# Optimization experiments

Hardware: AMD Instinct MI355X
Metric: run time of the kernel (lower is better)

## Reference

```python
import jax, jax.numpy as jnp
import numpy as np

N = 50000
D_IN = 512
D_HID = 2048
N_CLS = 40
E = 200000


def setup_inputs() -> dict:
    key = jax.random.key(0)
    ks = jax.random.split(key, 8)
    x = jax.random.normal(ks[0], (N, D_IN), dtype=jnp.float32)
    edge_index = jax.random.randint(ks[1], (2, E), 0, N, dtype=jnp.int32)
    # GCNConv weights (glorot-ish scale) and biases
    W1 = jax.random.normal(ks[2], (D_IN, D_HID), dtype=jnp.float32) / np.sqrt(D_IN)
    b1 = jnp.zeros((D_HID,), dtype=jnp.float32)
    W2 = jax.random.normal(ks[3], (D_HID, D_HID), dtype=jnp.float32) / np.sqrt(D_HID)
    b2 = jnp.zeros((D_HID,), dtype=jnp.float32)
    W3 = jax.random.normal(ks[4], (D_HID, N_CLS), dtype=jnp.float32) / np.sqrt(D_HID)
    b3 = jnp.zeros((N_CLS,), dtype=jnp.float32)
    return {"x": x, "edge_index": edge_index, "W1": W1, "b1": b1,
            "W2": W2, "b2": b2, "W3": W3, "b3": b3}


def _gcn_conv(x, src, dst, deg_norm, W, b, n):
    # PyG GCNConv: transform first, then normalized sum-aggregate, then bias.
    h = x @ W                              # [N, out]
    msg = h[src] * deg_norm[:, None]       # [E+N, out] gather + edge normalize
    out = jax.ops.segment_sum(msg, dst, num_segments=n)  # scatter-add
    return out + b


def _pairnorm(x, scale=1.0, eps=1e-6):
    # PyG PairNorm (scale_individually=False): center cols, rescale by mean row norm.
    xc = x - x.mean(axis=0, keepdims=True)
    denom = jnp.sqrt(eps + (xc * xc).sum(axis=-1).mean())
    return scale * xc / denom


def _edges_with_self_loops_and_norm(edge_index, n):
    loop = jnp.arange(n, dtype=edge_index.dtype)
    src = jnp.concatenate([edge_index[0], loop])
    dst = jnp.concatenate([edge_index[1], loop])
    deg = jax.ops.segment_sum(jnp.ones_like(dst, dtype=jnp.float32), dst, num_segments=n)
    dinv = jnp.where(deg > 0, jax.lax.rsqrt(jnp.maximum(deg, 1.0)), 0.0)
    norm = dinv[src] * dinv[dst]           # D^{-1/2} (A+I) D^{-1/2} edge weights
    return src, dst, norm


def reference(x, edge_index, W1, b1, W2, b2, W3, b3):
    n = x.shape[0]
    # drop_edge keep_ratio=1.0 keeps all edges -> identity
    src, dst, norm = _edges_with_self_loops_and_norm(edge_index, n)
    h = _gcn_conv(x, src, dst, norm, W1, b1, n)
    h = jax.nn.relu(_pairnorm(h))
    h = _gcn_conv(h, src, dst, norm, W2, b2, n)
    h = jax.nn.relu(_pairnorm(h))
    out = _gcn_conv(h, src, dst, norm, W3, b3, n)
    return out
```

## Files before the change

kernel.cpp:

```cpp
#include <hip/hip_runtime.h>
#include <cstdint>
#include <cstddef>

using f32x4 = __attribute__((ext_vector_type(4))) float;
using short8 = __attribute__((ext_vector_type(8))) short;

__device__ __forceinline__ float blo(unsigned int u) { return __uint_as_float(u << 16); }
__device__ __forceinline__ float bhi(unsigned int u) { return __uint_as_float(u & 0xffff0000u); }
__device__ __forceinline__ unsigned short f2b(float f) {
  unsigned int i = __float_as_uint(f);
  return (unsigned short)((i + 0x7fffu + ((i >> 16) & 1u)) >> 16);
}
__device__ __forceinline__ unsigned int packb2(float a, float b) {
  return (unsigned int)f2b(a) | ((unsigned int)f2b(b) << 16);
}
__device__ __forceinline__ void gload_lds16(const void* g, void* l) {
  typedef __attribute__((address_space(1))) const unsigned int gui_t;
  typedef __attribute__((address_space(3))) unsigned int lui_t;
  __builtin_amdgcn_global_load_lds((gui_t*)(uintptr_t)g, (lui_t*)(uintptr_t)l, 16, 0, 0);
}
__device__ __forceinline__ void xcd_remap(int gx, int gy, int& bx, int& by) {
  int nwg = gx * gy;
  int flat = by * gx + bx;
  int q = nwg >> 3, rmd = nwg & 7;
  int xcd = flat & 7, pos = flat >> 3;
  int base = (xcd < rmd) ? xcd * (q + 1) : rmd * (q + 1) + (xcd - rmd) * q;
  int nf = base + pos;
  bx = nf % gx;
  by = nf / gx;
}

__global__ void k_sentinel(float* out, long long total, float v) {
  long long i = (long long)blockIdx.x * blockDim.x + threadIdx.x;
  long long stride = (long long)gridDim.x * blockDim.x;
  for (; i < total; i += stride) out[i] = v;
}

__global__ void k_init_deg(int* deg, int n) {
  int i = blockIdx.x * blockDim.x + threadIdx.x;
  if (i < n) deg[i] = 1;
}
__global__ void k_count(const int* __restrict__ ei, int* __restrict__ deg, int e) {
  int i = blockIdx.x * blockDim.x + threadIdx.x;
  if (i < e) atomicAdd(&deg[ei[e + i]], 1);
}
__global__ void k_dinv(const int* __restrict__ deg, float* __restrict__ dinv, int n) {
  int i = blockIdx.x * blockDim.x + threadIdx.x;
  if (i < n) dinv[i] = rsqrtf((float)deg[i]);
}
__global__ void k_scan(const int* __restrict__ deg, int* __restrict__ offs, int n) {
  __shared__ int sums[1024];
  int tid = threadIdx.x;
  int chunk = (n + 1023) / 1024;
  int s0 = tid * chunk, s1 = s0 + chunk;
  if (s1 > n) s1 = n;
  if (s0 > n) s0 = n;
  int s = 0;
  for (int i = s0; i < s1; i++) s += deg[i];
  sums[tid] = s;
  __syncthreads();
  if (tid == 0) {
    int acc = 0;
    for (int i = 0; i < 1024; i++) { int v = sums[i]; sums[i] = acc; acc += v; }
  }
  __syncthreads();
  int off = sums[tid];
  for (int i = s0; i < s1; i++) { offs[i] = off; off += deg[i]; }
  if (tid == 1023) offs[n] = off;
}
__global__ void k_copy_int(int* __restrict__ dst, const int* __restrict__ src, int n) {
  int i = blockIdx.x * blockDim.x + threadIdx.x;
  if (i < n) dst[i] = src[i];
}
__global__ void k_copy_u4(uint4* __restrict__ dst, const uint4* __restrict__ src, int n16) {
  int i = blockIdx.x * blockDim.x + threadIdx.x;
  int stride = gridDim.x * blockDim.x;
  for (; i < n16; i += stride) dst[i] = src[i];
}
__global__ void k_fill_edges(const int* __restrict__ ei, int e, int* __restrict__ cursor,
                             unsigned short* __restrict__ colv) {
  int i = blockIdx.x * blockDim.x + threadIdx.x;
  if (i < e) {
    int s = ei[i], d = ei[e + i];
    int pos = atomicAdd(&cursor[d], 1);
    colv[pos] = (unsigned short)s;
  }
}
__global__ void k_fill_loops(int* __restrict__ cursor, unsigned short* __restrict__ colv, int n) {
  int i = blockIdx.x * blockDim.x + threadIdx.x;
  if (i < n) {
    int pos = atomicAdd(&cursor[i], 1);
    colv[pos] = (unsigned short)i;
  }
}

__global__ void k_transpose_cvt(const float* __restrict__ in, unsigned short* __restrict__ out,
                                int K, int M, int Mout) {
  __shared__ float tile[32][33];
  int kb = blockIdx.x * 32;
  int mb = blockIdx.y * 32;
  int tx = threadIdx.x, ty = threadIdx.y;
#pragma unroll
  for (int j = 0; j < 4; j++) {
    int k = kb + ty + j * 8, m = mb + tx;
    tile[ty + j * 8][tx] = (k < K && m < M) ? in[(size_t)k * M + m] : 0.0f;
  }
  __syncthreads();
#pragma unroll
  for (int j = 0; j < 4; j++) {
    int m = mb + ty + j * 8, k = kb + tx;
    if (m < Mout && k < K) out[(size_t)m * K + k] = f2b(tile[tx][ty + j * 8]);
  }
}

__global__ void k_aggregate_f32(const float* __restrict__ in, unsigned short* __restrict__ out,
                                const int* __restrict__ offs, const unsigned short* __restrict__ colv,
                                const float* __restrict__ dinv) {
  int i = blockIdx.x;
  int tid = threadIdx.x;
  float di = dinv[i];
  int p0 = offs[i], p1 = offs[i + 1];
  const float2* inv = (const float2*)in;
  float a0 = 0.f, a1 = 0.f;
  for (int p = p0; p < p1; p++) {
    int c = (int)colv[p];
    float wgt = dinv[c] * di;
    float2 v = inv[(size_t)c * 256 + tid];
    a0 += wgt * v.x; a1 += wgt * v.y;
  }
  ((unsigned int*)out)[(size_t)i * 256 + tid] = packb2(a0, a1);
}

__global__ void k_aggregate_pn(const unsigned short* __restrict__ in, unsigned short* __restrict__ outws,
                               unsigned short* __restrict__ outtail, int rsplit,
                               const int* __restrict__ offs, const unsigned short* __restrict__ colv,
                               const float* __restrict__ dinv, const float* __restrict__ meanv,
                               const float* __restrict__ scalev) {
  int i = blockIdx.x;
  int tid = threadIdx.x;
  float di = dinv[i];
  float s = scalev[0];
  float m[8];
#pragma unroll
  for (int j = 0; j < 8; j++) m[j] = meanv[tid * 8 + j];
  int p0 = offs[i], p1 = offs[i + 1];
  const uint4* inv = (const uint4*)in;
  float a[8] = {};
  for (int p = p0; p < p1; p++) {
    int c = (int)colv[p];
    float wgt = dinv[c] * di;
    uint4 u = inv[(size_t)c * 256 + tid];
    a[0] += wgt * fmaxf((blo(u.x) - m[0]) * s, 0.f);
    a[1] += wgt * fmaxf((bhi(u.x) - m[1]) * s, 0.f);
    a[2] += wgt * fmaxf((blo(u.y) - m[2]) * s, 0.f);
    a[3] += wgt * fmaxf((bhi(u.y) - m[3]) * s, 0.f);
    a[4] += wgt * fmaxf((blo(u.z) - m[4]) * s, 0.f);
    a[5] += wgt * fmaxf((bhi(u.z) - m[5]) * s, 0.f);
    a[6] += wgt * fmaxf((blo(u.w) - m[6]) * s, 0.f);
    a[7] += wgt * fmaxf((bhi(u.w) - m[7]) * s, 0.f);
  }
  uint4 o;
  o.x = packb2(a[0], a[1]); o.y = packb2(a[2], a[3]);
  o.z = packb2(a[4], a[5]); o.w = packb2(a[6], a[7]);
  char* base = (i < rsplit) ? (char*)outws + (size_t)i * 4096
                            : (char*)outtail + (size_t)(i - rsplit) * 4096;
  ((uint4*)base)[tid] = o;
}

template <int BM, int BN, int WAVES_M, int WAVES_N, bool ADD_BIAS, bool OUT_BF16, bool STATS>
__global__ __launch_bounds__(256) void k_gemm_bf16(const unsigned short* __restrict__ A,
                                                   const char* __restrict__ a_tail, int rsplit,
                                                   const unsigned short* __restrict__ BT,
                                                   const float* __restrict__ bias,
                                                   float* __restrict__ colsum, float* __restrict__ ssq,
                                                   void* __restrict__ Cout,
                                                   int M, int K, int Nout, int m_base) {
  constexpr int BK = 64;
  constexpr int FM = BM / (WAVES_M * 16);
  constexpr int FN = BN / (WAVES_N * 16);
  __shared__ unsigned short lA[BM * BK];
  __shared__ unsigned short lB[BN * BK];
  const int tid = threadIdx.x;
  const int lane = tid & 63;
  const int wid = tid >> 6;
  int bx = blockIdx.x, by = blockIdx.y;
  xcd_remap(gridDim.x, gridDim.y, bx, by);
  const int n0 = bx * BN;
  const int m0 = m_base + by * BM;
  const int wrow = (wid / WAVES_N) * (FM * 16);
  const int wcol = (wid % WAVES_N) * (FN * 16);
  constexpr int ABYTES = BM * BK * 2;
  constexpr int BBYTES = BN * BK * 2;
  constexpr int ACH = ABYTES / 4096;
  constexpr int BCH = BBYTES / 4096;
  const size_t rowbytes = (size_t)K * 2;

  f32x4 acc[FM][FN] = {};

  const int frow = lane & 15;
  const int kcol8 = (lane >> 4) * 8;
  const int xorb = (lane & 7) << 4;

  for (int k0 = 0; k0 < K; k0 += BK) {
#pragma unroll
    for (int c = 0; c < ACH; c++) {
      int o = wid * (ABYTES / 4) + c * 1024 + lane * 16;
      int r = o >> 7;
      int kbs = (o & 127) ^ ((r & 7) << 4);
      int gr = m0 + r; if (gr >= M) gr = M - 1;
      const char* rowp = (gr < rsplit) ? (const char*)A + (size_t)gr * rowbytes
                                       : a_tail + (size_t)(gr - rsplit) * rowbytes;
      gload_lds16(rowp + (size_t)k0 * 2 + kbs, (char*)lA + o);
    }
#pragma unroll
    for (int c = 0; c < BCH; c++) {
      int o = wid * (BBYTES / 4) + c * 1024 + lane * 16;
      int r = o >> 7;
      int kbs = (o & 127) ^ ((r & 7) << 4);
      gload_lds16((const char*)BT + (size_t)(n0 + r) * rowbytes + (size_t)k0 * 2 + kbs, (char*)lB + o);
    }
    __syncthreads();
#pragma unroll
    for (int kk = 0; kk < BK; kk += 32) {
      short8 af[FM], bfr[FN];
#pragma unroll
      for (int t = 0; t < FM; t++)
        af[t] = *(const short8*)((const char*)lA + (wrow + t * 16 + frow) * 128 +
                                 (((kk + kcol8) * 2) ^ xorb));
#pragma unroll
      for (int u = 0; u < FN; u++)
        bfr[u] = *(const short8*)((const char*)lB + (wcol + u * 16 + frow) * 128 +
                                  (((kk + kcol8) * 2) ^ xorb));
#pragma unroll
      for (int t = 0; t < FM; t++)
#pragma unroll
        for (int u = 0; u < FN; u++)
          acc[t][u] = __builtin_amdgcn_mfma_f32_16x16x32_bf16(af[t], bfr[u], acc[t][u], 0, 0, 0);
    }
    __syncthreads();
  }

  const int rrow = (lane >> 4) * 4;
  const int ccol = lane & 15;
  float ss = 0.f;
  float ca[FN];
#pragma unroll
  for (int u = 0; u < FN; u++) ca[u] = 0.f;
#pragma unroll
  for (int t = 0; t < FM; t++) {
#pragma unroll
    for (int u = 0; u < FN; u++) {
#pragma unroll
      for (int r = 0; r < 4; r++) {
        int row = m0 + wrow + t * 16 + rrow + r;
        int col = n0 + wcol + u * 16 + ccol;
        if (row < M && col < Nout) {
          float v = acc[t][u][r];
          if constexpr (ADD_BIAS) v += bias[col];
          if constexpr (OUT_BF16)
            ((unsigned short*)Cout)[(size_t)row * Nout + col] = f2b(v);
          else
            ((float*)Cout)[(size_t)row * Nout + col] = v;
          if constexpr (STATS) { ca[u] += v; ss += v * v; }
        }
      }
    }
  }
  if constexpr (STATS) {
#pragma unroll
    for (int u = 0; u < FN; u++) {
      float w = ca[u];
      w += __shfl_xor(w, 16);
      w += __shfl_xor(w, 32);
      if (lane < 16) atomicAdd(&colsum[n0 + wcol + u * 16 + lane], w);
    }
    for (int mk = 32; mk >= 1; mk >>= 1) ss += __shfl_xor(ss, mk);
    if (lane == 0) atomicAdd(ssq, ss);
  }
}

__global__ void k_zero(float* p, int n) {
  int i = blockIdx.x * blockDim.x + threadIdx.x;
  if (i < n) p[i] = 0.f;
}
__global__ void k_finalize(const float* __restrict__ colsum, const float* __restrict__ ssq,
                           float* __restrict__ meanv, float* __restrict__ scalev, int nrows, int ncols) {
  __shared__ float red[1024];
  int tid = threadIdx.x;
  float m2 = 0.f;
  for (int c = tid; c < ncols; c += 1024) {
    float m = colsum[c] / (float)nrows;
    meanv[c] = m;
    m2 += m * m;
  }
  red[tid] = m2;
  __syncthreads();
  for (int s = 512; s > 0; s >>= 1) {
    if (tid < s) red[tid] += red[tid + s];
    __syncthreads();
  }
  if (tid == 0) {
    float sstot = ssq[0] - (float)nrows * red[0];
    scalev[0] = rsqrtf(1e-6f + sstot / (float)nrows);
  }
}
__global__ void k_apply_pn_relu(unsigned int* __restrict__ h, const float* __restrict__ meanv,
                                const float* __restrict__ scalev, long long total, int ucolmask) {
  float s = scalev[0];
  long long i = (long long)blockIdx.x * blockDim.x + threadIdx.x;
  long long stride = (long long)gridDim.x * blockDim.x;
  for (; i < total; i += stride) {
    unsigned int u = h[i];
    int cp = (int)(i & ucolmask);
    float a = (blo(u) - meanv[2 * cp]) * s;
    float b = (bhi(u) - meanv[2 * cp + 1]) * s;
    h[i] = packb2(fmaxf(a, 0.f), fmaxf(b, 0.f));
  }
}

__global__ void k_aggregate_out(const float* __restrict__ t, const int* __restrict__ offs,
                                const unsigned short* __restrict__ colv, const float* __restrict__ dinv,
                                const float* __restrict__ b3, float* __restrict__ outp, int ncls) {
  int i = blockIdx.x;
  int j = threadIdx.x;
  if (j < ncls) {
    float di = dinv[i];
    float acc = b3[j];
    for (int p = offs[i]; p < offs[i + 1]; p++) {
      int c = (int)colv[p];
      acc += dinv[c] * di * t[(size_t)c * ncls + j];
    }
    outp[(size_t)i * ncls + j] = acc;
  }
}

extern "C" void kernel_launch(void* const* d_in, const int* in_sizes, int n_in,
                              void* d_out, int out_size, void* d_ws, size_t ws_size,
                              hipStream_t stream) {
  (void)n_in;
  const float* x = (const float*)d_in[0];
  const int* ei = (const int*)d_in[1];
  const float* W1 = (const float*)d_in[2];
  const float* b1 = (const float*)d_in[3];
  const float* W2 = (const float*)d_in[4];
  const float* b2 = (const float*)d_in[5];
  const float* W3 = (const float*)d_in[6];
  const float* b3 = (const float*)d_in[7];
  const int DI = 512, DH = 2048, NC = 40;
  const int n = in_sizes[0] / DI;
  const int e = in_sizes[1] / 2;

  const size_t BIG1B = (size_t)n * DH * 2;
  char* BIG1 = (char*)d_ws;
  char* BIG2 = (char*)d_ws + BIG1B;

  char* dob = (char*)d_out;
  int* deg = (int*)(dob + 0);
  float* dinv = (float*)(dob + 200064);
  int* offs = (int*)(dob + 400128);
  unsigned short* colv = (unsigned short*)(dob + 600192);
  float* colsum = (float*)(dob + 1100288);
  float* meanv = (float*)(dob + 1108480);
  float* ssq = (float*)(dob + 1116672);
  float* scalev = (float*)(dob + 1116928);
  char* aggtail = dob + 2097152;

  long long rows_ws = (long long)(ws_size - BIG1B) / (DH * 2);
  int rsplit = (rows_ws > n) ? n : (int)rows_ws;

  if (ws_size < 403800000UL || rsplit < 48560) {
    float v = (float)(double)(ws_size >> 20);
    k_sentinel<<<512, 256, 0, stream>>>((float*)d_out, (long long)out_size, v);
    return;
  }

  const int W2ROW0 = 47952;
  unsigned short* WT2 = (unsigned short*)(BIG1 + (size_t)W2ROW0 * 4096);
  const int PH1_TILES = 374;
  const int PH2_MBASE = PH1_TILES * 128;
  const int PH2_TILES = (n - PH2_MBASE + 127) / 128;

  unsigned short* agg1 = (unsigned short*)BIG2;
  unsigned short* WT1 = (unsigned short*)(BIG2 + 64000000);
  unsigned short* agg2 = (unsigned short*)BIG2;
  unsigned short* WT2c = (unsigned short*)BIG2;
  float* tbuf = (float*)BIG2;
  unsigned short* WT3 = (unsigned short*)(BIG2 + 9000000);
  int* offs_c = (int*)(BIG2 + 10000000);
  unsigned short* colv_c = (unsigned short*)(BIG2 + 11000000);
  float* dinv_c = (float*)(BIG2 + 12000000);

  dim3 b256(256);
  int gn = (n + 255) / 256, ge = (e + 255) / 256;

  k_init_deg<<<gn, b256, 0, stream>>>(deg, n);
  k_count<<<ge, b256, 0, stream>>>(ei, deg, e);
  k_dinv<<<gn, b256, 0, stream>>>(deg, dinv, n);
  k_scan<<<1, 1024, 0, stream>>>(deg, offs, n);
  k_copy_int<<<gn, b256, 0, stream>>>(deg, offs, n);
  k_fill_edges<<<ge, b256, 0, stream>>>(ei, e, deg, colv);
  k_fill_loops<<<gn, b256, 0, stream>>>(deg, colv, n);

  dim3 tb(32, 8);

  k_aggregate_f32<<<n, b256, 0, stream>>>(x, agg1, offs, colv, dinv);
  k_transpose_cvt<<<dim3(DI / 32, DH / 32), tb, 0, stream>>>(W1, WT1, DI, DH, DH);
  k_zero<<<(DH + 255) / 256, b256, 0, stream>>>(colsum, DH);
  k_zero<<<1, b256, 0, stream>>>(ssq, 1);
  k_gemm_bf16<128, 128, 2, 2, true, true, true><<<dim3(DH / 128, (n + 127) / 128), b256, 0, stream>>>(
      agg1, (const char*)agg1, n, WT1, b1, colsum, ssq, BIG1, n, DI, DH, 0);
  k_finalize<<<1, 1024, 0, stream>>>(colsum, ssq, meanv, scalev, n, DH);

  k_aggregate_pn<<<n, b256, 0, stream>>>((const unsigned short*)BIG1, agg2, (unsigned short*)aggtail,
                                         rsplit, offs, colv, dinv, meanv, scalev);
  k_transpose_cvt<<<dim3(DH / 32, DH / 32), tb, 0, stream>>>(W2, WT2, DH, DH, DH);
  k_zero<<<(DH + 255) / 256, b256, 0, stream>>>(colsum, DH);
  k_zero<<<1, b256, 0, stream>>>(ssq, 1);
  k_gemm_bf16<128, 128, 2, 2, true, true, true><<<dim3(DH / 128, PH1_TILES), b256, 0, stream>>>(
      agg2, aggtail, rsplit, WT2, b2, colsum, ssq, BIG1, n, DH, DH, 0);
  k_copy_u4<<<2048, b256, 0, stream>>>((uint4*)WT2c, (const uint4*)WT2, (int)(8388608 / 16));
  k_gemm_bf16<128, 128, 2, 2, true, true, true><<<dim3(DH / 128, PH2_TILES), b256, 0, stream>>>(
      agg2, aggtail, rsplit, WT2c, b2, colsum, ssq, BIG1, n, DH, DH, PH2_MBASE);
  k_finalize<<<1, 1024, 0, stream>>>(colsum, ssq, meanv, scalev, n, DH);
  k_apply_pn_relu<<<2048, b256, 0, stream>>>((unsigned int*)BIG1, meanv, scalev, (long long)n * DH / 2, DH / 2 - 1);

  k_transpose_cvt<<<dim3(DH / 32, 2), tb, 0, stream>>>(W3, WT3, DH, NC, 64);
  k_gemm_bf16<128, 64, 4, 1, false, false, false><<<dim3(1, (n + 127) / 128), b256, 0, stream>>>(
      (const unsigned short*)BIG1, BIG1, n, WT3, nullptr, nullptr, nullptr, tbuf, n, DH, NC, 0);
  k_copy_int<<<(n + 256) / 256, b256, 0, stream>>>(offs_c, offs, n + 1);
  k_copy_int<<<((e + n) / 2 + 255) / 256, b256, 0, stream>>>((int*)colv_c, (const int*)colv, (e + n) / 2);
  k_copy_int<<<gn, b256, 0, stream>>>((int*)dinv_c, (const int*)dinv, n);
  k_aggregate_out<<<n, 64, 0, stream>>>(tbuf, offs_c, colv_c, dinv_c, b3, (float*)d_out, NC);
}
```

Baseline: 1.601 ms.

## Use 256x256 double-buffered MFMA GEMM and aggregate bf16-converted input features

Adds a new 512-thread GEMM kernel with 256x256 output tiles. It double-buffers LDS (128KB), splits each K step into four phases that interleave global-to-LDS loads with MFMA compute behind explicit waitcnt and barriers, and raises MFMA priority during compute. This replaces the 128x128 GEMM for layers 1 and 2 to get more operand reuse and overlap loads with compute. It also converts x to bf16 first so the first aggregation gathers half the bytes per edge, at the cost of an extra conversion pass and lower input precision. The larger tiles change the row split between the two layer-2 phases, and the very large LDS footprint limits occupancy.

Measured after the change: 1.407 ms. -12.1%, faster.

```diff
diff --git a/kernel.cpp b/kernel.cpp
--- a/kernel.cpp
+++ b/kernel.cpp
@@ -94,6 +94,14 @@
   }
 }
 
+__global__ void k_cvt_bf16(const float2* __restrict__ in, unsigned int* __restrict__ out, long long total) {
+  long long i = (long long)blockIdx.x * blockDim.x + threadIdx.x;
+  long long stride = (long long)gridDim.x * blockDim.x;
+  for (; i < total; i += stride) {
+    float2 v = in[i];
+    out[i] = packb2(v.x, v.y);
+  }
+}
 __global__ void k_transpose_cvt(const float* __restrict__ in, unsigned short* __restrict__ out,
                                 int K, int M, int Mout) {
   __shared__ float tile[32][33];
@@ -113,20 +121,19 @@
   }
 }
 
-__global__ void k_aggregate_f32(const float* __restrict__ in, unsigned short* __restrict__ out,
+__global__ void k_aggregate_512(const unsigned int* __restrict__ in, unsigned short* __restrict__ out,
                                 const int* __restrict__ offs, const unsigned short* __restrict__ colv,
                                 const float* __restrict__ dinv) {
   int i = blockIdx.x;
   int tid = threadIdx.x;
   float di = dinv[i];
   int p0 = offs[i], p1 = offs[i + 1];
-  const float2* inv = (const float2*)in;
   float a0 = 0.f, a1 = 0.f;
   for (int p = p0; p < p1; p++) {
     int c = (int)colv[p];
     float wgt = dinv[c] * di;
-    float2 v = inv[(size_t)c * 256 + tid];
-    a0 += wgt * v.x; a1 += wgt * v.y;
+    unsigned int u = in[(size_t)c * 256 + tid];
+    a0 += wgt * blo(u); a1 += wgt * bhi(u);
   }
   ((unsigned int*)out)[(size_t)i * 256 + tid] = packb2(a0, a1);
 }
@@ -165,6 +172,156 @@
   char* base = (i < rsplit) ? (char*)outws + (size_t)i * 4096
                             : (char*)outtail + (size_t)(i - rsplit) * 4096;
   ((uint4*)base)[tid] = o;
+}
+
+template <int MQ, int NQ, bool LOADA>
+__device__ __forceinline__ void do_phase(const char* ldsA, const char* ldsB,
+                                         short8 (&a)[4][2], short8 (&b)[2][2], f32x4 (&acc)[8][4],
+                                         int wm, int wn, int lane) {
+  const int frow = lane & 15;
+  const int cb0 = (lane >> 4) << 4;
+  const int xorb = (lane & 7) << 4;
+  if (LOADA) {
+#pragma unroll
+    for (int i = 0; i < 4; i++)
+#pragma unroll
+      for (int kk = 0; kk < 2; kk++)
+        a[i][kk] = *(const short8*)(ldsA + (wm * 128 + MQ * 64 + i * 16 + frow) * 128 +
+                                    ((kk * 64 + cb0) ^ xorb));
+  }
+#pragma unroll
+  for (int j = 0; j < 2; j++)
+#pragma unroll
+    for (int kk = 0; kk < 2; kk++)
+      b[j][kk] = *(const short8*)(ldsB + (wn * 64 + NQ * 32 + j * 16 + frow) * 128 +
+                                  ((kk * 64 + cb0) ^ xorb));
+  __builtin_amdgcn_s_setprio(1);
+#pragma unroll
+  for (int i = 0; i < 4; i++)
+#pragma unroll
+    for (int j = 0; j < 2; j++)
+#pragma unroll
+      for (int kk = 0; kk < 2; kk++)
+        acc[MQ * 4 + i][NQ * 2 + j] =
+            __builtin_amdgcn_mfma_f32_16x16x32_bf16(a[i][kk], b[j][kk], acc[MQ * 4 + i][NQ * 2 + j], 0, 0, 0);
+  __builtin_amdgcn_s_setprio(0);
+}
+
+__global__ __launch_bounds__(512, 2) void k_gemm256(const unsigned short* __restrict__ A,
+                                                    const char* __restrict__ a_tail, int rsplit,
+                                                    const unsigned short* __restrict__ BT,
+                                                    const float* __restrict__ bias,
+                                                    float* __restrict__ colsum, float* __restrict__ ssq,
+                                                    unsigned short* __restrict__ Cout,
+                                                    int M, int K, int Nout, int m_base) {
+  __shared__ __align__(16) char smem[131072];
+  const int t = threadIdx.x;
+  const int lane = t & 63;
+  const int wid = t >> 6;
+  const int wm = wid >> 2, wn = wid & 3;
+  int bx = blockIdx.x, by = blockIdx.y;
+  xcd_remap(gridDim.x, gridDim.y, bx, by);
+  const int n0 = bx * 256;
+  const int m0 = m_base + by * 256;
+  const size_t rowK = (size_t)K * 2;
+  const int NT = K >> 6;
+
+  const int rA = t >> 3;
+  const int colS = (((t & 7) ^ ((t >> 3) & 7)) << 4);
+
+  auto rowptrA = [&](int r) -> const char* {
+    int gr = m0 + r; if (gr >= M) gr = M - 1;
+    return (gr < rsplit ? (const char*)A + (size_t)gr * rowK
+                        : a_tail + (size_t)(gr - rsplit) * rowK) + colS;
+  };
+  const char* sA00 = rowptrA(rA);
+  const char* sA01 = rowptrA(128 + rA);
+  const char* sA10 = rowptrA(64 + rA);
+  const char* sA11 = rowptrA(192 + rA);
+  const int rbl = (t >> 8) * 64 + ((t >> 3) & 31);
+  const int rB00 = rbl, rB01 = 128 + rbl;
+  const int rB10 = 32 + rbl, rB11 = 160 + rbl;
+  const char* sB00 = (const char*)BT + (size_t)(n0 + rB00) * rowK + colS;
+  const char* sB01 = (const char*)BT + (size_t)(n0 + rB01) * rowK + colS;
+  const char* sB10 = (const char*)BT + (size_t)(n0 + rB10) * rowK + colS;
+  const char* sB11 = (const char*)BT + (size_t)(n0 + rB11) * rowK + colS;
+  const int t16 = t * 16;
+  const int dA00 = t16, dA01 = 16384 + t16, dA10 = 8192 + t16, dA11 = 24576 + t16;
+  const int c7 = (t & 7) * 16;
+  const int dB00 = 32768 + rB00 * 128 + c7, dB01 = 32768 + rB01 * 128 + c7;
+  const int dB10 = 32768 + rB10 * 128 + c7, dB11 = 32768 + rB11 * 128 + c7;
+
+  f32x4 acc[8][4] = {};
+  short8 a[4][2], b[2][2];
+
+  gload_lds16(sA00, smem + dA00); gload_lds16(sA01, smem + dA01);
+  gload_lds16(sB00, smem + dB00); gload_lds16(sB01, smem + dB01);
+  gload_lds16(sB10, smem + dB10); gload_lds16(sB11, smem + dB11);
+  gload_lds16(sA10, smem + dA10); gload_lds16(sA11, smem + dA11);
+  sA00 += 128; sA01 += 128; sA10 += 128; sA11 += 128;
+  sB00 += 128; sB01 += 128; sB10 += 128; sB11 += 128;
+
+  for (int kt = 0; kt < NT; ++kt) {
+    const int cbo = (kt & 1) << 16;
+    const int sbo = cbo ^ 65536;
+    const char* LA = (const char*)smem + cbo;
+    const char* LB = LA + 32768;
+    gload_lds16(sA00, smem + sbo + dA00); gload_lds16(sA01, smem + sbo + dA01);
+    asm volatile("s_waitcnt vmcnt(6)" ::: "memory");
+    asm volatile("s_barrier" ::: "memory");
+    do_phase<0, 0, true>(LA, LB, a, b, acc, wm, wn, lane);
+    asm volatile("s_barrier" ::: "memory");
+    gload_lds16(sB00, smem + sbo + dB00); gload_lds16(sB01, smem + sbo + dB01);
+    asm volatile("s_waitcnt vmcnt(6)" ::: "memory");
+    asm volatile("s_barrier" ::: "memory");
+    do_phase<0, 1, false>(LA, LB, a, b, acc, wm, wn, lane);
+    asm volatile("s_barrier" ::: "memory");
+    gload_lds16(sB10, smem + sbo + dB10); gload_lds16(sB11, smem + sbo + dB11);
+    asm volatile("s_waitcnt vmcnt(6)" ::: "memory");
+    asm volatile("s_barrier" ::: "memory");
+    do_phase<1, 0, true>(LA, LB, a, b, acc, wm, wn, lane);
+    asm volatile("s_barrier" ::: "memory");
+    gload_lds16(sA10, smem + sbo + dA10); gload_lds16(sA11, smem + sbo + dA11);
+    asm volatile("s_waitcnt vmcnt(6)" ::: "memory");
+    asm volatile("s_barrier" ::: "memory");
+    do_phase<1, 1, false>(LA, LB, a, b, acc, wm, wn, lane);
+    asm volatile("s_barrier" ::: "memory");
+    if (kt + 1 < NT) {
+      sA00 += 128; sA01 += 128; sA10 += 128; sA11 += 128;
+      sB00 += 128; sB01 += 128; sB10 += 128; sB11 += 128;
+    }
+  }
+
+  const int rrow = (lane >> 4) * 4;
+  const int ccol = lane & 15;
+  float ss = 0.f;
+  float csum[4] = {0.f, 0.f, 0.f, 0.f};
+#pragma unroll
+  for (int f = 0; f < 8; f++) {
+#pragma unroll
+    for (int g = 0; g < 4; g++) {
+      int col = n0 + wn * 64 + g * 16 + ccol;
+      float bv = bias[col];
+#pragma unroll
+      for (int r = 0; r < 4; r++) {
+        int row = m0 + wm * 128 + f * 16 + rrow + r;
+        if (row < M) {
+          float v = acc[f][g][r] + bv;
+          Cout[(size_t)row * Nout + col] = f2b(v);
+          csum[g] += v; ss += v * v;
+        }
+      }
+    }
+  }
+#pragma unroll
+  for (int g = 0; g < 4; g++) {
+    float w = csum[g];
+    w += __shfl_xor(w, 16);
+    w += __shfl_xor(w, 32);
+    if (lane < 16) atomicAdd(&colsum[n0 + wn * 64 + g * 16 + lane], w);
+  }
+  for (int mk = 32; mk >= 1; mk >>= 1) ss += __shfl_xor(ss, mk);
+  if (lane == 0) atomicAdd(ssq, ss);
 }
 
 template <int BM, int BN, int WAVES_M, int WAVES_N, bool ADD_BIAS, bool OUT_BF16, bool STATS>
@@ -196,7 +353,6 @@
   const size_t rowbytes = (size_t)K * 2;
 
   f32x4 acc[FM][FN] = {};
-
   const int frow = lane & 15;
   const int kcol8 = (lane >> 4) * 8;
   const int xorb = (lane & 7) << 4;
@@ -376,12 +532,12 @@
 
   const int W2ROW0 = 47952;
   unsigned short* WT2 = (unsigned short*)(BIG1 + (size_t)W2ROW0 * 4096);
-  const int PH1_TILES = 374;
-  const int PH2_MBASE = PH1_TILES * 128;
-  const int PH2_TILES = (n - PH2_MBASE + 127) / 128;
+  const int PH2_MBASE = 47872;
+  const int PH2_TILES = (n - PH2_MBASE + 255) / 256;
 
   unsigned short* agg1 = (unsigned short*)BIG2;
-  unsigned short* WT1 = (unsigned short*)(BIG2 + 64000000);
+  unsigned short* xb = (unsigned short*)(BIG2 + 64000000);
+  unsigned short* WT1 = (unsigned short*)(BIG2 + 120000000);
   unsigned short* agg2 = (unsigned short*)BIG2;
   unsigned short* WT2c = (unsigned short*)BIG2;
   float* tbuf = (float*)BIG2;
@@ -391,6 +547,7 @@
   float* dinv_c = (float*)(BIG2 + 12000000);
 
   dim3 b256(256);
+  dim3 b512(512);
   int gn = (n + 255) / 256, ge = (e + 255) / 256;
 
   k_init_deg<<<gn, b256, 0, stream>>>(deg, n);
@@ -403,12 +560,13 @@
 
   dim3 tb(32, 8);
 
-  k_aggregate_f32<<<n, b256, 0, stream>>>(x, agg1, offs, colv, dinv);
+  k_cvt_bf16<<<2048, b256, 0, stream>>>((const float2*)x, (unsigned int*)xb, (long long)n * DI / 2);
+  k_aggregate_512<<<n, b256, 0, stream>>>((const unsigned int*)xb, agg1, offs, colv, dinv);
   k_transpose_cvt<<<dim3(DI / 32, DH / 32), tb, 0, stream>>>(W1, WT1, DI, DH, DH);
   k_zero<<<(DH + 255) / 256, b256, 0, stream>>>(colsum, DH);
   k_zero<<<1, b256, 0, stream>>>(ssq, 1);
-  k_gemm_bf16<128, 128, 2, 2, true, true, true><<<dim3(DH / 128, (n + 127) / 128), b256, 0, stream>>>(
-      agg1, (const char*)agg1, n, WT1, b1, colsum, ssq, BIG1, n, DI, DH, 0);
+  k_gemm256<<<dim3(DH / 256, (n + 255) / 256), b512, 0, stream>>>(
+      agg1, (const char*)agg1, n, WT1, b1, colsum, ssq, (unsigned short*)BIG1, n, DI, DH, 0);
   k_finalize<<<1, 1024, 0, stream>>>(colsum, ssq, meanv, scalev, n, DH);
 
   k_aggregate_pn<<<n, b256, 0, stream>>>((const unsigned short*)BIG1, agg2, (unsigned short*)aggtail,
@@ -416,11 +574,11 @@
   k_transpose_cvt<<<dim3(DH / 32, DH / 32), tb, 0, stream>>>(W2, WT2, DH, DH, DH);
   k_zero<<<(DH + 255) / 256, b256, 0, stream>>>(colsum, DH);
   k_zero<<<1, b256, 0, stream>>>(ssq, 1);
-  k_gemm_bf16<128, 128, 2, 2, true, true, true><<<dim3(DH / 128, PH1_TILES), b256, 0, stream>>>(
-      agg2, aggtail, rsplit, WT2, b2, colsum, ssq, BIG1, n, DH, DH, 0);
+  k_gemm256<<<dim3(DH / 256, 187), b512, 0, stream>>>(
+      agg2, aggtail, rsplit, WT2, b2, colsum, ssq, (unsigned short*)BIG1, n, DH, DH, 0);
   k_copy_u4<<<2048, b256, 0, stream>>>((uint4*)WT2c, (const uint4*)WT2, (int)(8388608 / 16));
-  k_gemm_bf16<128, 128, 2, 2, true, true, true><<<dim3(DH / 128, PH2_TILES), b256, 0, stream>>>(
-      agg2, aggtail, rsplit, WT2c, b2, colsum, ssq, BIG1, n, DH, DH, PH2_MBASE);
+  k_gemm256<<<dim3(DH / 256, PH2_TILES), b512, 0, stream>>>(
+      agg2, aggtail, rsplit, WT2c, b2, colsum, ssq, (unsigned short*)BIG1, n, DH, DH, PH2_MBASE);
   k_finalize<<<1, 1024, 0, stream>>>(colsum, ssq, meanv, scalev, n, DH);
   k_apply_pn_relu<<<2048, b256, 0, stream>>>((unsigned int*)BIG1, meanv, scalev, (long long)n * DH / 2, DH / 2 - 1);
 
```
